# Kernel optimization log

Measured on AMD Instinct MI355X. Metric: run time of the kernel, lower is better.

The kernel has to match this reference:

```python
import jax, jax.numpy as jnp
import numpy as np

B, N, IN_DIM, HID, OUT_DIM, CODEBOOK = 32, 2048, 128, 64, 64, 2048


def setup_inputs() -> dict:
    key = jax.random.key(0)
    ks = jax.random.split(key, 6)
    # xavier-uniform-ish scales for the MLP weights
    def xavier(k, fan_in, fan_out):
        gain = float(np.sqrt(2.0))  # relu gain
        lim = gain * np.sqrt(6.0 / (fan_in + fan_out))
        return jax.random.uniform(k, (fan_in, fan_out), jnp.float32, -lim, lim)
    return {
        "obs": jax.random.normal(ks[0], (B, N, IN_DIM), jnp.float32),
        "W1": xavier(ks[1], IN_DIM, HID),
        "b1": jnp.full((HID,), 0.01, jnp.float32),
        "W2": xavier(ks[2], HID, HID),
        "b2": jnp.full((HID,), 0.01, jnp.float32),
        "W3": xavier(ks[3], HID, OUT_DIM),
        "b3": jnp.full((OUT_DIM,), 0.01, jnp.float32),
        "codebook": jax.random.normal(ks[4], (CODEBOOK, OUT_DIM), jnp.float32),
    }


def reference(obs, W1, b1, W2, b2, W3, b3, codebook):
    # --- tiny MLP ---
    h = jax.nn.relu(obs @ W1 + b1)
    h = jax.nn.relu(h @ W2 + b2)
    x = h @ W3 + b3  # [B, N, D]

    # --- vector quantize: euclidean nearest codebook entry ---
    x2 = jnp.sum(x * x, axis=-1, keepdims=True)           # [B, N, 1]
    e2 = jnp.sum(codebook * codebook, axis=-1)            # [C]
    dist = x2 - 2.0 * jnp.einsum("bnd,cd->bnc", x, codebook) + e2  # [B, N, C]
    idx = jnp.argmin(dist, axis=-1)                        # [B, N] int
    quantize = codebook[idx]                               # [B, N, D] gather

    # commitment loss: mse(sg(quantize), x)
    cmt_loss = jnp.mean((jax.lax.stop_gradient(quantize) - x) ** 2)
    # straight-through estimator
    msg = x + jax.lax.stop_gradient(quantize - x)
    return (msg, idx, cmt_loss)
```

## Files before the change

### kernel.cpp

```cpp
#include <hip/hip_runtime.h>


#define NPTS    65536
#define IN_DIM  128
#define HID     64
#define OUT_DIM 64
#define CB_N    2048
#define MSG_ELEMS (NPTS * OUT_DIM)
#define LOSS_SCALE (1.0f / 4194304.0f)
#define MARG 0.5f
#define CAND_CAP 1024
#define BPTS 128
#define NTHR 512

typedef __attribute__((ext_vector_type(8))) short short8;
typedef _Float16 half8 __attribute__((ext_vector_type(8)));
typedef __attribute__((ext_vector_type(4))) float f32x4;
typedef unsigned int u32;
typedef unsigned long long u64;

__device__ __forceinline__ void gld16(void* lds_base, const void* gsrc) {
    __builtin_amdgcn_global_load_lds(
        (const __attribute__((address_space(1))) u32*)gsrc,
        (__attribute__((address_space(3))) u32*)lds_base, 16, 0, 0);
}

__global__ __launch_bounds__(256) void prep_all(
    const float* __restrict__ cb,
    const float* __restrict__ W1, const float* __restrict__ W2,
    const float* __restrict__ W3,
    float* __restrict__ e2,
    _Float16* __restrict__ cbh,
    _Float16* __restrict__ w1h, _Float16* __restrict__ w1l,
    _Float16* __restrict__ w2h, _Float16* __restrict__ w2l,
    _Float16* __restrict__ w3h, _Float16* __restrict__ w3l,
    float* __restrict__ loss)
{
    const int b = blockIdx.x, tid = threadIdx.x;
    if (b < 64) {
        const int id = b * 256 + tid;
        const int n = id >> 3, h = (id >> 2) & 1, quad = id & 3;
        const int t = n >> 4, l15 = n & 15;
        const float* src = cb + (long)n * OUT_DIM + h * 32 + quad * 8;
        half8 hi;
        #pragma unroll
        for (int j = 0; j < 8; ++j)
            hi[j] = (_Float16)src[j];
        const long dst = ((long)(t * 2 + h) * 64 + quad * 16 + l15) * 8;
        *(half8*)(cbh + dst) = hi;
    } else if (b < 72) {
        const int id = (b - 64) * 256 + tid;
        const int lane = id & 63;
        const int m = lane & 15, quad = lane >> 4;
        const float* W; _Float16 *dh, *dl; int frag;
        if (id < 1024)      { W = W1; dh = w1h; dl = w1l; frag = id >> 6; }
        else if (id < 1536) { W = W2; dh = w2h; dl = w2l; frag = (id - 1024) >> 6; }
        else                { W = W3; dh = w3h; dl = w3l; frag = (id - 1536) >> 6; }
        const int kc = frag >> 2, nt = frag & 3;
        half8 hi, lo;
        #pragma unroll
        for (int j = 0; j < 8; ++j) {
            const float v = W[(long)(kc * 32 + quad * 8 + j) * 64 + nt * 16 + m];
            hi[j] = (_Float16)v;
            lo[j] = (_Float16)(v - (float)hi[j]);
        }
        const long dst = (long)(frag * 64 + lane) * 8;
        *(half8*)(dh + dst) = hi;
        *(half8*)(dl + dst) = lo;
    } else {
        if (b == 72 && tid == 0) *loss = 0.0f;
        const int c = (b - 72) * 256 + tid;
        const float4* row = (const float4*)(cb + (long)c * OUT_DIM);
        float s = 0.0f;
        #pragma unroll
        for (int mq = 0; mq < 16; ++mq) {
            const float4 v = row[mq];
            s += v.x * v.x + v.y * v.y + v.z * v.z + v.w * v.w;
        }
        e2[c] = s;
    }
}

#define MFMA16(A, B, C) __builtin_amdgcn_mfma_f32_16x16x32_f16(A, B, C, 0, 0, 0)

__device__ __forceinline__ void split16(const float* xs, half8& h, half8& l) {
    #pragma unroll
    for (int j = 0; j < 8; ++j) {
        h[j] = (_Float16)xs[j];
        l[j] = (_Float16)(xs[j] - (float)h[j]);
    }
}

__device__ __forceinline__ u64 packkey(float d, int n) {
    u32 ub = __float_as_uint(d);
    ub = (ub & 0x80000000u) ? ~ub : (ub | 0x80000000u);
    return ((u64)ub << 32) | (u32)n;
}

__device__ __forceinline__ float exdist(
    const float* xr, const float* __restrict__ cbrow, float e2v)
{
    const float4* xp = (const float4*)xr;
    const float4* cp = (const float4*)cbrow;
    float a0 = 0.0f, a1 = 0.0f;
    #pragma unroll
    for (int mq = 0; mq < 16; ++mq) {
        const float4 xv = xp[mq], cv = cp[mq];
        a0 = fmaf(xv.x, cv.x, a0); a1 = fmaf(xv.y, cv.y, a1);
        a0 = fmaf(xv.z, cv.z, a0); a1 = fmaf(xv.w, cv.w, a1);
    }
    return fmaf(-2.0f, a0 + a1, e2v);
}

__global__ __launch_bounds__(NTHR, 4) void fused_mlp_vq(
    const float* __restrict__ obs,
    const float* __restrict__ b1, const float* __restrict__ b2,
    const float* __restrict__ b3,
    const _Float16* __restrict__ w1h, const _Float16* __restrict__ w1l,
    const _Float16* __restrict__ w2h, const _Float16* __restrict__ w2l,
    const _Float16* __restrict__ w3h, const _Float16* __restrict__ w3l,
    const float* __restrict__ cb,
    const _Float16* __restrict__ cbhp,
    const float* __restrict__ e2,
    float* __restrict__ msg,
    float* __restrict__ idx_out,
    float* __restrict__ loss_out)
{
    __shared__ float hbuf[BPTS * 68];
    __shared__ __align__(16) char stg[2][16384];
    __shared__ int   cand_pc[CAND_CAP];
    __shared__ u64   keys[BPTS];
    __shared__ int   win_sh[BPTS];
    __shared__ int   idx_sh[BPTS];
    __shared__ float wred[NTHR / 64];
    __shared__ int   cand_cnt;

    const int t = threadIdx.x, lane = t & 63, w = t >> 6;
    const int m = lane & 15, quad = lane >> 4;
    const long base = (long)blockIdx.x * BPTS;
    const int row0 = w * 16 + quad * 4;
    const int arow_l = w * 16 + m;

    if (t == 0) cand_cnt = 0;
    if (t < BPTS) keys[t] = ~0ULL;

    {
        float bb1[4], bb2[4], bb3[4];
        #pragma unroll
        for (int nt = 0; nt < 4; ++nt) {
            bb1[nt] = b1[nt * 16 + m];
            bb2[nt] = b2[nt * 16 + m];
            bb3[nt] = b3[nt * 16 + m];
        }

        const float* arow = obs + (base + w * 16 + m) * IN_DIM;
        half8 a1h[4], a1l[4];
        #pragma unroll
        for (int kc = 0; kc < 4; ++kc) {
            const float4 va = *(const float4*)(arow + kc * 32 + quad * 8);
            const float4 vb = *(const float4*)(arow + kc * 32 + quad * 8 + 4);
            const float xs[8] = {va.x, va.y, va.z, va.w, vb.x, vb.y, vb.z, vb.w};
            split16(xs, a1h[kc], a1l[kc]);
        }

        #pragma unroll
        for (int nt = 0; nt < 4; ++nt) {
            f32x4 acc = {0.0f, 0.0f, 0.0f, 0.0f};
            #pragma unroll
            for (int kc = 0; kc < 4; ++kc) {
                const long fo = (long)((kc * 4 + nt) * 64 + lane) * 8;
                const half8 wh = *(const half8*)(w1h + fo);
                const half8 wl = *(const half8*)(w1l + fo);
                acc = MFMA16(a1h[kc], wh, acc);
                acc = MFMA16(a1l[kc], wh, acc);
                acc = MFMA16(a1h[kc], wl, acc);
            }
            #pragma unroll
            for (int r = 0; r < 4; ++r) {
                const float v = acc[r] + bb1[nt];
                hbuf[(row0 + r) * 68 + nt * 16 + m] = v > 0.0f ? v : 0.0f;
            }
        }

        half8 a2h[2], a2l[2];
        #pragma unroll
        for (int kc = 0; kc < 2; ++kc) {
            const float4 va = *(const float4*)&hbuf[arow_l * 68 + kc * 32 + quad * 8];
            const float4 vb = *(const float4*)&hbuf[arow_l * 68 + kc * 32 + quad * 8 + 4];
            const float xs[8] = {va.x, va.y, va.z, va.w, vb.x, vb.y, vb.z, vb.w};
            split16(xs, a2h[kc], a2l[kc]);
        }
        #pragma unroll
        for (int nt = 0; nt < 4; ++nt) {
            f32x4 acc = {0.0f, 0.0f, 0.0f, 0.0f};
            #pragma unroll
            for (int kc = 0; kc < 2; ++kc) {
                const long fo = (long)((kc * 4 + nt) * 64 + lane) * 8;
                const half8 wh = *(const half8*)(w2h + fo);
                const half8 wl = *(const half8*)(w2l + fo);
                acc = MFMA16(a2h[kc], wh, acc);
                acc = MFMA16(a2l[kc], wh, acc);
                acc = MFMA16(a2h[kc], wl, acc);
            }
            #pragma unroll
            for (int r = 0; r < 4; ++r) {
                const float v = acc[r] + bb2[nt];
                hbuf[(row0 + r) * 68 + nt * 16 + m] = v > 0.0f ? v : 0.0f;
            }
        }

        half8 a3h[2], a3l[2];
        #pragma unroll
        for (int kc = 0; kc < 2; ++kc) {
            const float4 va = *(const float4*)&hbuf[arow_l * 68 + kc * 32 + quad * 8];
            const float4 vb = *(const float4*)&hbuf[arow_l * 68 + kc * 32 + quad * 8 + 4];
            const float xs[8] = {va.x, va.y, va.z, va.w, vb.x, vb.y, vb.z, vb.w};
            split16(xs, a3h[kc], a3l[kc]);
        }
        #pragma unroll
        for (int nt = 0; nt < 4; ++nt) {
            f32x4 acc = {0.0f, 0.0f, 0.0f, 0.0f};
            #pragma unroll
            for (int kc = 0; kc < 2; ++kc) {
                const long fo = (long)((kc * 4 + nt) * 64 + lane) * 8;
                const half8 wh = *(const half8*)(w3h + fo);
                const half8 wl = *(const half8*)(w3l + fo);
                acc = MFMA16(a3h[kc], wh, acc);
                acc = MFMA16(a3l[kc], wh, acc);
                acc = MFMA16(a3h[kc], wl, acc);
            }
            #pragma unroll
            for (int r = 0; r < 4; ++r)
                hbuf[(row0 + r) * 68 + nt * 16 + m] = acc[r] + bb3[nt];
        }
    }

    half8 a0h, a1h;
    {
        const float* xrow = &hbuf[(w * 16 + m) * 68];
        const float4 xa = *(const float4*)(xrow + quad * 8);
        const float4 xb = *(const float4*)(xrow + quad * 8 + 4);
        const float4 xc = *(const float4*)(xrow + 32 + quad * 8);
        const float4 xd = *(const float4*)(xrow + 32 + quad * 8 + 4);
        const float x0[8] = {xa.x, xa.y, xa.z, xa.w, xb.x, xb.y, xb.z, xb.w};
        const float x1[8] = {xc.x, xc.y, xc.z, xc.w, xd.x, xd.y, xd.z, xd.w};
        #pragma unroll
        for (int j = 0; j < 8; ++j) {
            a0h[j] = (_Float16)x0[j];
            a1h[j] = (_Float16)x1[j];
        }
    }

    #pragma unroll
    for (int j = 0; j < 2; ++j)
        gld16(stg[0] + (w * 2 + j) * 1024,
              cbhp + (w * 2 + j) * 512 + lane * 8);
    __syncthreads();

    float bd[4] = {3.4e38f, 3.4e38f, 3.4e38f, 3.4e38f};
    int   bi[4] = {0, 0, 0, 0};

    for (int ph = 0; ph < 16; ++ph) {
        if (ph < 15) {
            const _Float16* cbq = cbhp + (long)(ph + 1) * 8192;
            #pragma unroll
            for (int j = 0; j < 2; ++j)
                gld16(stg[(ph + 1) & 1] + (w * 2 + j) * 1024,
                      cbq + (w * 2 + j) * 512 + lane * 8);
        }
        const char* bufp = stg[ph & 1];
        #pragma unroll
        for (int tl = 0; tl < 8; ++tl) {
            const int g = ph * 8 + tl;
            const half8 th0 = *(const half8*)(bufp + tl * 2048 + lane * 16);
            const half8 th1 = *(const half8*)(bufp + tl * 2048 + 1024 + lane * 16);
            const float e2v = e2[g * 16 + m];
            f32x4 acc = {0.0f, 0.0f, 0.0f, 0.0f};
            __builtin_amdgcn_s_setprio(1);
            acc = MFMA16(a0h, th0, acc);
            acc = MFMA16(a1h, th1, acc);
            __builtin_amdgcn_s_setprio(0);

            const int code = g * 16 + m;
            bool pushm[4]; int pip[4];
            #pragma unroll
            for (int r = 0; r < 4; ++r) {
                const float d = fmaf(-2.0f, acc[r], e2v);
                const bool lt = d < bd[r];
                pushm[r] = __builtin_fabsf(d - bd[r]) < MARG;
                pip[r] = lt ? bi[r] : code;
                bd[r] = lt ? d : bd[r];
                bi[r] = lt ? code : bi[r];
            }
            if (__any((int)(pushm[0] | pushm[1] | pushm[2] | pushm[3]))) {
                #pragma unroll
                for (int r = 0; r < 4; ++r) {
                    if (pushm[r]) {
                        const int slot = atomicAdd(&cand_cnt, 1);
                        if (slot < CAND_CAP)
                            cand_pc[slot] = ((w * 16 + quad * 4 + r) << 16) | pip[r];
                    }
                }
            }
        }
        __syncthreads();
    }

    {
        float rd[4]; int ri[4];
        #pragma unroll
        for (int r = 0; r < 4; ++r) { rd[r] = bd[r]; ri[r] = bi[r]; }
        #pragma unroll
        for (int off = 1; off <= 8; off <<= 1) {
            #pragma unroll
            for (int r = 0; r < 4; ++r) {
                const float od = __shfl_xor(rd[r], off, 64);
                const int   oi = __shfl_xor(ri[r], off, 64);
                if (od < rd[r] || (od == rd[r] && oi < ri[r])) {
                    rd[r] = od; ri[r] = oi;
                }
            }
        }
        #pragma unroll
        for (int r = 0; r < 4; ++r) {
            const int pl = w * 16 + quad * 4 + r;
            if (m == 0) win_sh[pl] = ri[r];
            if (bd[r] <= rd[r] + MARG && bi[r] != ri[r]) {
                const int slot = atomicAdd(&cand_cnt, 1);
                if (slot < CAND_CAP)
                    cand_pc[slot] = (pl << 16) | bi[r];
            }
        }
    }
    __syncthreads();

    {
        if (t < BPTS) {
            const int n = win_sh[t];
            const float ex = exdist(&hbuf[t * 68], cb + (long)n * OUT_DIM, e2[n]);
            atomicMin(&keys[t], packkey(ex, n));
        }
        const int L = min(cand_cnt, CAND_CAP);
        for (int l = t; l < L; l += NTHR) {
            const int pc = cand_pc[l];
            const int p = pc >> 16, n = pc & 0xFFFF;
            const float ex = exdist(&hbuf[p * 68], cb + (long)n * OUT_DIM, e2[n]);
            atomicMin(&keys[p], packkey(ex, n));
        }
    }
    __syncthreads();

    if (t < BPTS) {
        const int code = (int)(keys[t] & 0xFFFFFFFFu);
        idx_sh[t] = code;
        idx_out[base + t] = (float)code;
    }
    __syncthreads();

    float lsum = 0.0f;
    float4* mg = (float4*)(msg + base * OUT_DIM);
    #pragma unroll
    for (int mm = 0; mm < 4; ++mm) {
        const int v = t + NTHR * mm;
        const int p = v >> 4, k4 = v & 15;
        const int code = idx_sh[p];
        const float4 q = ((const float4*)(cb + (long)code * OUT_DIM))[k4];
        const float4 xv = *(const float4*)&hbuf[p * 68 + k4 * 4];
        const float dx = q.x - xv.x, dy = q.y - xv.y;
        const float dz = q.z - xv.z, dw2 = q.w - xv.w;
        lsum += dx * dx + dy * dy + dz * dz + dw2 * dw2;
        mg[v] = q;
    }
    #pragma unroll
    for (int off = 32; off > 0; off >>= 1) lsum += __shfl_down(lsum, off, 64);
    if (lane == 0) wred[w] = lsum;
    __syncthreads();
    if (t == 0) {
        float s = 0.0f;
        #pragma unroll
        for (int i = 0; i < NTHR / 64; ++i) s += wred[i];
        atomicAdd(loss_out, s * LOSS_SCALE);
    }
}

extern "C" void kernel_launch(void* const* d_in, const int* in_sizes, int n_in,
                              void* d_out, int out_size, void* d_ws, size_t ws_size,
                              hipStream_t stream) {
    const float* obs = (const float*)d_in[0];
    const float* W1  = (const float*)d_in[1];
    const float* b1  = (const float*)d_in[2];
    const float* W2  = (const float*)d_in[3];
    const float* b2  = (const float*)d_in[4];
    const float* W3  = (const float*)d_in[5];
    const float* b3  = (const float*)d_in[6];
    const float* cb  = (const float*)d_in[7];

    float* out  = (float*)d_out;
    float* msg  = out;
    float* idxf = out + MSG_ELEMS;
    float* loss = out + MSG_ELEMS + NPTS;

    char* ws = (char*)d_ws;
    float*     e2  = (float*)ws;
    _Float16*  cbh = (_Float16*)(ws + 8192);
    _Float16* w1h = (_Float16*)(ws + 532480);
    _Float16* w1l = (_Float16*)(ws + 548864);
    _Float16* w2h = (_Float16*)(ws + 565248);
    _Float16* w2l = (_Float16*)(ws + 573440);
    _Float16* w3h = (_Float16*)(ws + 581632);
    _Float16* w3l = (_Float16*)(ws + 589824);

    prep_all<<<80, 256, 0, stream>>>(cb, W1, W2, W3, e2, cbh,
                                     w1h, w1l, w2h, w2l, w3h, w3l, loss);
    fused_mlp_vq<<<NPTS / BPTS, NTHR, 0, stream>>>(
        obs, b1, b2, b3, w1h, w1l, w2h, w2l, w3h, w3l,
        cb, cbh, e2, msg, idxf, loss);
}
```

Before: 159.6 us.

## Switch codebook staging to per-wave triple-buffered rings without block barriers

Replaces the block-shared double-buffered codebook staging, which needed a __syncthreads per phase, with a private three-slot ring per wave. Each slot is fetched via global_load_lds and waited on with an explicit vmcnt. The block shrinks to 64 points and 256 threads, and the squared codebook norms are cached in LDS. The aim is to remove block-wide synchronization stalls in the argmin loop. The cost is that every wave streams the whole codebook itself, which multiplies L2 codebook traffic.

```diff
diff --git a/kernel.cpp b/kernel.cpp
--- a/kernel.cpp
+++ b/kernel.cpp
@@ -9,9 +9,9 @@
 #define MSG_ELEMS (NPTS * OUT_DIM)
 #define LOSS_SCALE (1.0f / 4194304.0f)
 #define MARG 0.5f
-#define CAND_CAP 1024
-#define BPTS 128
-#define NTHR 512
+#define CAND_CAP 512
+#define BPTS 64
+#define NTHR 256
 
 typedef __attribute__((ext_vector_type(8))) short short8;
 typedef _Float16 half8 __attribute__((ext_vector_type(8)));
@@ -127,7 +127,8 @@
     float* __restrict__ loss_out)
 {
     __shared__ float hbuf[BPTS * 68];
-    __shared__ __align__(16) char stg[2][16384];
+    __shared__ float e2s[CB_N];
+    __shared__ __align__(16) char stg[4][3][2048];
     __shared__ int   cand_pc[CAND_CAP];
     __shared__ u64   keys[BPTS];
     __shared__ int   win_sh[BPTS];
@@ -143,6 +144,8 @@
 
     if (t == 0) cand_cnt = 0;
     if (t < BPTS) keys[t] = ~0ULL;
+    ((float4*)e2s)[t * 2]     = ((const float4*)e2)[t * 2];
+    ((float4*)e2s)[t * 2 + 1] = ((const float4*)e2)[t * 2 + 1];
 
     {
         float bb1[4], bb2[4], bb3[4];
@@ -250,60 +253,61 @@
             a1h[j] = (_Float16)x1[j];
         }
     }
-
-    #pragma unroll
-    for (int j = 0; j < 2; ++j)
-        gld16(stg[0] + (w * 2 + j) * 1024,
-              cbhp + (w * 2 + j) * 512 + lane * 8);
     __syncthreads();
 
     float bd[4] = {3.4e38f, 3.4e38f, 3.4e38f, 3.4e38f};
     int   bi[4] = {0, 0, 0, 0};
 
-    for (int ph = 0; ph < 16; ++ph) {
-        if (ph < 15) {
-            const _Float16* cbq = cbhp + (long)(ph + 1) * 8192;
-            #pragma unroll
-            for (int j = 0; j < 2; ++j)
-                gld16(stg[(ph + 1) & 1] + (w * 2 + j) * 1024,
-                      cbq + (w * 2 + j) * 512 + lane * 8);
-        }
-        const char* bufp = stg[ph & 1];
-        #pragma unroll
-        for (int tl = 0; tl < 8; ++tl) {
-            const int g = ph * 8 + tl;
-            const half8 th0 = *(const half8*)(bufp + tl * 2048 + lane * 16);
-            const half8 th1 = *(const half8*)(bufp + tl * 2048 + 1024 + lane * 16);
-            const float e2v = e2[g * 16 + m];
-            f32x4 acc = {0.0f, 0.0f, 0.0f, 0.0f};
-            __builtin_amdgcn_s_setprio(1);
-            acc = MFMA16(a0h, th0, acc);
-            acc = MFMA16(a1h, th1, acc);
-            __builtin_amdgcn_s_setprio(0);
-
-            const int code = g * 16 + m;
-            bool pushm[4]; int pip[4];
+    char* ring = stg[w][0];
+    const long lofs = (long)lane * 8;
+
+    #pragma unroll
+    for (int tl = 0; tl < 2; ++tl) {
+        gld16(ring + tl * 2048,        cbhp + (long)tl * 1024 + lofs);
+        gld16(ring + tl * 2048 + 1024, cbhp + (long)tl * 1024 + 512 + lofs);
+    }
+
+    for (int tile = 0; tile < 128; ++tile) {
+        {
+            const int nt = (tile + 2 < 128) ? tile + 2 : 127;
+            char* dst = ring + ((tile + 2) % 3) * 2048;
+            gld16(dst,        cbhp + (long)nt * 1024 + lofs);
+            gld16(dst + 1024, cbhp + (long)nt * 1024 + 512 + lofs);
+        }
+        asm volatile("s_waitcnt vmcnt(4)" ::: "memory");
+        __builtin_amdgcn_sched_barrier(0);
+
+        const char* bufp = ring + (tile % 3) * 2048;
+        const half8 th0 = *(const half8*)(bufp + lane * 16);
+        const half8 th1 = *(const half8*)(bufp + 1024 + lane * 16);
+        const float e2v = e2s[tile * 16 + m];
+        f32x4 acc = {0.0f, 0.0f, 0.0f, 0.0f};
+        __builtin_amdgcn_s_setprio(1);
+        acc = MFMA16(a0h, th0, acc);
+        acc = MFMA16(a1h, th1, acc);
+        __builtin_amdgcn_s_setprio(0);
+
+        const int code = tile * 16 + m;
+        bool pushm[4]; int pip[4];
+        #pragma unroll
+        for (int r = 0; r < 4; ++r) {
+            const float d = fmaf(-2.0f, acc[r], e2v);
+            const bool lt = d < bd[r];
+            pushm[r] = __builtin_fabsf(d - bd[r]) < MARG;
+            pip[r] = lt ? bi[r] : code;
+            bd[r] = lt ? d : bd[r];
+            bi[r] = lt ? code : bi[r];
+        }
+        if (__any((int)(pushm[0] | pushm[1] | pushm[2] | pushm[3]))) {
             #pragma unroll
             for (int r = 0; r < 4; ++r) {
-                const float d = fmaf(-2.0f, acc[r], e2v);
-                const bool lt = d < bd[r];
-                pushm[r] = __builtin_fabsf(d - bd[r]) < MARG;
-                pip[r] = lt ? bi[r] : code;
-                bd[r] = lt ? d : bd[r];
-                bi[r] = lt ? code : bi[r];
-            }
-            if (__any((int)(pushm[0] | pushm[1] | pushm[2] | pushm[3]))) {
-                #pragma unroll
-                for (int r = 0; r < 4; ++r) {
-                    if (pushm[r]) {
-                        const int slot = atomicAdd(&cand_cnt, 1);
-                        if (slot < CAND_CAP)
-                            cand_pc[slot] = ((w * 16 + quad * 4 + r) << 16) | pip[r];
-                    }
+                if (pushm[r]) {
+                    const int slot = atomicAdd(&cand_cnt, 1);
+                    if (slot < CAND_CAP)
+                        cand_pc[slot] = ((w * 16 + quad * 4 + r) << 16) | pip[r];
                 }
             }
         }
-        __syncthreads();
     }
 
     {
@@ -337,14 +341,14 @@
     {
         if (t < BPTS) {
             const int n = win_sh[t];
-            const float ex = exdist(&hbuf[t * 68], cb + (long)n * OUT_DIM, e2[n]);
+            const float ex = exdist(&hbuf[t * 68], cb + (long)n * OUT_DIM, e2s[n]);
             atomicMin(&keys[t], packkey(ex, n));
         }
         const int L = min(cand_cnt, CAND_CAP);
         for (int l = t; l < L; l += NTHR) {
             const int pc = cand_pc[l];
             const int p = pc >> 16, n = pc & 0xFFFF;
-            const float ex = exdist(&hbuf[p * 68], cb + (long)n * OUT_DIM, e2[n]);
+            const float ex = exdist(&hbuf[p * 68], cb + (long)n * OUT_DIM, e2s[n]);
             atomicMin(&keys[p], packkey(ex, n));
         }
     }
```

Result: slower. 223.0 us (+39.7%).
